# Kernel optimization log

Measured on AMD Instinct MI355X. Metric: run time of the kernel, lower is better.

## Reference

```python
import jax, jax.numpy as jnp
import numpy as np

DIM = 1024
NUM_HEAD = 16
N_IMG = 64


def _linear_params(key, scale=0.02):
    kw, kb = jax.random.split(key)
    W = jax.random.normal(kw, (DIM, DIM), jnp.float32) * scale
    b = jax.random.normal(kb, (DIM,), jnp.float32) * scale
    return W, b


def setup_inputs() -> dict:
    key = jax.random.key(0)
    ks = jax.random.split(key, 5)
    # ragged per-image instance counts: 128..254, deterministic, sum = 12224
    lens = (128 + 2 * np.arange(N_IMG)).astype(np.int64)
    N = int(lens.sum())  # 12224
    x = jax.random.normal(ks[0], (N, DIM), jnp.float32)
    Wq, bq = _linear_params(ks[1])
    Wk, bk = _linear_params(ks[2])
    Wv, bv = _linear_params(ks[3])
    Wu, bu = _linear_params(ks[4])
    return {"x": x, "Wq": Wq, "bq": bq, "Wk": Wk, "bk": bk,
            "Wv": Wv, "bv": bv, "Wu": Wu, "bu": bu,
            "num_inst_per_image": jnp.asarray(lens)}


def _segment_layout(num_inst_per_image):
    # static (int) metadata -> numpy; returns padded gather idx, key mask, unpad idx
    lens = np.asarray(num_inst_per_image)
    B = lens.shape[0]
    L = int(lens.max())
    offsets = np.concatenate([[0], np.cumsum(lens)[:-1]])
    pos = offsets[:, None] + np.arange(L)[None, :]           # [B, L] flat positions
    valid = np.arange(L)[None, :] < lens[:, None]            # [B, L]
    gather_idx = jnp.asarray(np.where(valid, pos, 0))        # safe gather
    flat_take = jnp.asarray(np.flatnonzero(valid.ravel()))   # [N] unpad (row-major = segment order)
    return gather_idx, jnp.asarray(valid), flat_take, B, L


def reference(x, Wq, bq, Wk, bk, Wv, bv, Wu, bu, num_inst_per_image):
    gather_idx, valid, flat_take, B, L = _segment_layout(num_inst_per_image)
    N, C = x.shape
    H = NUM_HEAD
    D = C // H
    # global QKV projections on the flat batch (as in the torch module)
    q = (x @ Wq + bq)[gather_idx].reshape(B, L, H, D)
    k = (x @ Wk + bk)[gather_idx].reshape(B, L, H, D)
    v = (x @ Wv + bv)[gather_idx].reshape(B, L, H, D)
    scale = 1.0 / np.sqrt(C)  # note: original divides by sqrt(C), not sqrt(head_dim)
    attn = jnp.einsum('bqhd,bkhd->bhqk', q, k) * scale       # [B, H, L, L]
    bias = jnp.where(valid[:, None, None, :], 0.0, -jnp.inf)  # mask padded keys
    attn = jax.nn.softmax(attn + bias, axis=-1)
    out = jnp.einsum('bhqk,bkhd->bqhd', attn, v).reshape(B * L, C)
    out = out[flat_take]                                      # unpad back to [N, C]
    return out @ Wu + bu
```

## Files before the change

### kernel.cpp

```cpp
#include <hip/hip_runtime.h>
#include <hip/hip_bf16.h>
#include <math.h>

#define DIMC 1024
#define NHEAD 16
#define HDIM 64
#define MPAD 12288

using bf16x8 = __attribute__((ext_vector_type(8))) short;
using f32x4  = __attribute__((ext_vector_type(4))) float;
using f32x16 = __attribute__((ext_vector_type(16))) float;

__device__ inline ushort f2bf(float f) {
    uint u = __float_as_uint(f);
    u += 0x7fffu + ((u >> 16) & 1u);
    return (ushort)(u >> 16);
}
__device__ inline float bf2f(ushort h) { return __uint_as_float(((uint)h) << 16); }

__device__ inline uint pkbf(float a, float b) {
    __hip_bfloat162 t = __float22bfloat162_rn(float2{a, b});
    return *reinterpret_cast<uint*>(&t);
}

__device__ inline void gload_lds16(const ushort* g, ushort* l) {
    __builtin_amdgcn_global_load_lds(
        (const __attribute__((address_space(1))) uint*)g,
        (__attribute__((address_space(3))) uint*)l, 16, 0, 0);
}

__global__ __launch_bounds__(512, 2) void gemm192(
    const ushort* __restrict__ A, const ushort* __restrict__ Bt,
    const float* __restrict__ bq, const float* __restrict__ bk,
    const float* __restrict__ bv,
    ushort* __restrict__ qb, ushort* __restrict__ kb, ushort* __restrict__ vb,
    int M)
{
    __shared__ ushort lds[2][(256 + 192) * 64];

    const int bid = blockIdx.x;
    const int xcd = bid & 7;
    const int j   = bid >> 3;
    const int mt  = xcd * 6 + (j % 6);
    const int nt  = j / 6;
    const int row0 = mt * 256;
    const int col0 = nt * 192;

    const int t512 = threadIdx.x;
    const int w    = t512 >> 6;
    const int lane = t512 & 63;
    const int wm   = w >> 2;
    const int wn   = w & 3;
    const int l15  = lane & 15;
    const int kh   = lane >> 4;

    auto stage = [&](int buf, int kt, int mat, int relRow) {
        const int o   = relRow * 128 + lane * 16;
        const int row = o >> 7;
        const int kb_ = (o & 127) ^ ((row & 7) << 4);
        const ushort* src = (mat ? Bt + (size_t)(col0 + row) * DIMC
                                 : A  + (size_t)(row0 + row) * DIMC)
                            + kt * 64 + (kb_ >> 1);
        gload_lds16(src, &lds[buf][0] + mat * (256 * 64) + relRow * 64);
    };
    auto rdA = [&](int buf, int qr, int fr, int ks) -> bf16x8 {
        const int row = wm * 128 + qr * 64 + fr * 16 + l15;
        const int ad  = (row * 128 + ks * 64 + kh * 16) ^ ((row & 7) << 4);
        return *(const bf16x8*)(&lds[buf][0] + (ad >> 1));
    };
    auto rdB = [&](int buf, int n, int ks) -> bf16x8 {
        const int row = wn * 48 + n * 16 + l15;
        const int ad  = (row * 128 + ks * 64 + kh * 16) ^ ((row & 7) << 4);
        return *(const bf16x8*)(&lds[buf][256 * 64] + (ad >> 1));
    };

    f32x4 acc[8][3] = {};
    bf16x8 af[4][2];
    bf16x8 bf[3][2];

    stage(0, 0, 0, wm * 128 + wn * 16);
    stage(0, 0, 0, wm * 128 + wn * 16 + 8);
    stage(0, 0, 1, wn * 48 + wm * 16);
    stage(0, 0, 1, wn * 48 + wm * 16 + 8);
    stage(0, 0, 1, wn * 48 + 32 + wm * 8);
    stage(0, 0, 0, wm * 128 + 64 + wn * 16);
    stage(0, 0, 0, wm * 128 + 64 + wn * 16 + 8);

    const int NT = DIMC / 64;
    for (int t = 0; t < NT; ++t) {
        const int cur = t & 1;
        const int nxt = cur ^ 1;
        const int tn  = (t + 1 < NT) ? (t + 1) : (NT - 1);

        asm volatile("s_waitcnt vmcnt(2)" ::: "memory");
        __builtin_amdgcn_s_barrier();
        __builtin_amdgcn_sched_barrier(0);
        #pragma unroll
        for (int fr = 0; fr < 4; ++fr)
            #pragma unroll
            for (int ks = 0; ks < 2; ++ks)
                af[fr][ks] = rdA(cur, 0, fr, ks);
        #pragma unroll
        for (int n = 0; n < 3; ++n)
            #pragma unroll
            for (int ks = 0; ks < 2; ++ks)
                bf[n][ks] = rdB(cur, n, ks);
        stage(nxt, tn, 0, wm * 128 + wn * 16);
        stage(nxt, tn, 0, wm * 128 + wn * 16 + 8);
        stage(nxt, tn, 1, wn * 48 + wm * 16);
        stage(nxt, tn, 1, wn * 48 + wm * 16 + 8);
        stage(nxt, tn, 1, wn * 48 + 32 + wm * 8);
        __builtin_amdgcn_s_setprio(1);
        #pragma unroll
        for (int fr = 0; fr < 4; ++fr)
            #pragma unroll
            for (int n = 0; n < 3; ++n)
                #pragma unroll
                for (int ks = 0; ks < 2; ++ks)
                    acc[fr][n] = __builtin_amdgcn_mfma_f32_16x16x32_bf16(
                        af[fr][ks], bf[n][ks], acc[fr][n], 0, 0, 0);
        __builtin_amdgcn_s_setprio(0);

        asm volatile("s_waitcnt vmcnt(5)" ::: "memory");
        __builtin_amdgcn_s_barrier();
        __builtin_amdgcn_sched_barrier(0);
        #pragma unroll
        for (int fr = 0; fr < 4; ++fr)
            #pragma unroll
            for (int ks = 0; ks < 2; ++ks)
                af[fr][ks] = rdA(cur, 1, fr, ks);
        stage(nxt, tn, 0, wm * 128 + 64 + wn * 16);
        stage(nxt, tn, 0, wm * 128 + 64 + wn * 16 + 8);
        __builtin_amdgcn_s_setprio(1);
        #pragma unroll
        for (int fr = 0; fr < 4; ++fr)
            #pragma unroll
            for (int n = 0; n < 3; ++n)
                #pragma unroll
                for (int ks = 0; ks < 2; ++ks)
                    acc[4 + fr][n] = __builtin_amdgcn_mfma_f32_16x16x32_bf16(
                        af[fr][ks], bf[n][ks], acc[4 + fr][n], 0, 0, 0);
        __builtin_amdgcn_s_setprio(0);
    }

    #pragma unroll
    for (int n = 0; n < 3; ++n) {
        const int cg = col0 + wn * 48 + n * 16 + l15;
        const int s  = cg >> 10;
        const int cb = cg & 1023;
        const float bb = ((s == 0) ? bq : (s == 1) ? bk : bv)[cb];
        ushort* op     = (s == 0) ? qb : (s == 1) ? kb : vb;
        #pragma unroll
        for (int i = 0; i < 8; ++i) {
            #pragma unroll
            for (int r = 0; r < 4; ++r) {
                const int gr = row0 + wm * 128 + i * 16 + kh * 4 + r;
                if (gr < M)
                    op[(size_t)gr * DIMC + cb] = f2bf(acc[i][n][r] + bb);
            }
        }
    }
}

__global__ __launch_bounds__(512, 2) void gemmF(
    const ushort* __restrict__ A, const ushort* __restrict__ Bt,
    const float* __restrict__ bias, float* __restrict__ C, int M)
{
    __shared__ ushort lds[2][(192 + 256) * 64];

    const int bid = blockIdx.x;
    const int xcd = bid & 7;
    const int j   = bid >> 3;
    const int mt  = xcd * 8 + (j % 8);
    const int nt  = j / 8;
    const int row0 = mt * 192;
    const int col0 = nt * 256;

    const int t512 = threadIdx.x;
    const int w    = t512 >> 6;
    const int lane = t512 & 63;
    const int wm   = w >> 2;
    const int wn   = w & 3;
    const int l15  = lane & 15;
    const int kh   = lane >> 4;

    const int awbase = (w & 4) ? (96 + (w - 4) * 8) : (w * 8);

    auto stage = [&](int buf, int kt, int mat, int relRow) {
        const int o   = relRow * 128 + lane * 16;
        const int row = o >> 7;
        const int kb_ = (o & 127) ^ ((row & 7) << 4);
        const ushort* src = (mat ? Bt + (size_t)(col0 + row) * DIMC
                                 : A  + (size_t)(row0 + row) * DIMC)
                            + kt * 64 + (kb_ >> 1);
        gload_lds16(src, &lds[buf][0] + mat * (192 * 64) + relRow * 64);
    };
    auto rdA = [&](int buf, int fr, int ks) -> bf16x8 {
        const int row = wm * 96 + fr * 16 + l15;
        const int ad  = (row * 128 + ks * 64 + kh * 16) ^ ((row & 7) << 4);
        return *(const bf16x8*)(&lds[buf][0] + (ad >> 1));
    };
    auto rdB = [&](int buf, int n, int ks) -> bf16x8 {
        const int row = wn * 64 + n * 16 + l15;
        const int ad  = (row * 128 + ks * 64 + kh * 16) ^ ((row & 7) << 4);
        return *(const bf16x8*)(&lds[buf][192 * 64] + (ad >> 1));
    };

    f32x4 acc[6][4] = {};
    bf16x8 af[2][2];
    bf16x8 bf[4][2];

    stage(0, 0, 1, w * 32);
    stage(0, 0, 1, w * 32 + 8);
    stage(0, 0, 1, w * 32 + 16);
    stage(0, 0, 1, w * 32 + 24);
    stage(0, 0, 0, awbase);
    stage(0, 0, 0, awbase + 32);
    stage(0, 0, 0, awbase + 64);

    const int NT = DIMC / 64;
    for (int t = 0; t < NT; ++t) {
        const int cur = t & 1;
        const int nxt = cur ^ 1;
        const int tn  = (t + 1 < NT) ? (t + 1) : (NT - 1);

        asm volatile("s_waitcnt vmcnt(2)" ::: "memory");
        __builtin_amdgcn_s_barrier();
        __builtin_amdgcn_sched_barrier(0);
        #pragma unroll
        for (int fr = 0; fr < 2; ++fr)
            #pragma unroll
            for (int ks = 0; ks < 2; ++ks)
                af[fr][ks] = rdA(cur, fr, ks);
        #pragma unroll
        for (int n = 0; n < 4; ++n)
            #pragma unroll
            for (int ks = 0; ks < 2; ++ks)
                bf[n][ks] = rdB(cur, n, ks);
        stage(nxt, tn, 1, w * 32);
        stage(nxt, tn, 1, w * 32 + 8);
        stage(nxt, tn, 1, w * 32 + 16);
        stage(nxt, tn, 1, w * 32 + 24);
        stage(nxt, tn, 0, awbase);
        __builtin_amdgcn_s_setprio(1);
        #pragma unroll
        for (int fr = 0; fr < 2; ++fr)
            #pragma unroll
            for (int n = 0; n < 4; ++n)
                #pragma unroll
                for (int ks = 0; ks < 2; ++ks)
                    acc[fr][n] = __builtin_amdgcn_mfma_f32_16x16x32_bf16(
                        af[fr][ks], bf[n][ks], acc[fr][n], 0, 0, 0);
        __builtin_amdgcn_s_setprio(0);

        asm volatile("s_waitcnt vmcnt(6)" ::: "memory");
        __builtin_amdgcn_s_barrier();
        __builtin_amdgcn_sched_barrier(0);
        #pragma unroll
        for (int fr = 0; fr < 2; ++fr)
            #pragma unroll
            for (int ks = 0; ks < 2; ++ks)
                af[fr][ks] = rdA(cur, 2 + fr, ks);
        stage(nxt, tn, 0, awbase + 32);
        __builtin_amdgcn_s_setprio(1);
        #pragma unroll
        for (int fr = 0; fr < 2; ++fr)
            #pragma unroll
            for (int n = 0; n < 4; ++n)
                #pragma unroll
                for (int ks = 0; ks < 2; ++ks)
                    acc[2 + fr][n] = __builtin_amdgcn_mfma_f32_16x16x32_bf16(
                        af[fr][ks], bf[n][ks], acc[2 + fr][n], 0, 0, 0);
        __builtin_amdgcn_s_setprio(0);

        asm volatile("s_waitcnt vmcnt(6)" ::: "memory");
        __builtin_amdgcn_s_barrier();
        __builtin_amdgcn_sched_barrier(0);
        #pragma unroll
        for (int fr = 0; fr < 2; ++fr)
            #pragma unroll
            for (int ks = 0; ks < 2; ++ks)
                af[fr][ks] = rdA(cur, 4 + fr, ks);
        stage(nxt, tn, 0, awbase + 64);
        __builtin_amdgcn_s_setprio(1);
        #pragma unroll
        for (int fr = 0; fr < 2; ++fr)
            #pragma unroll
            for (int n = 0; n < 4; ++n)
                #pragma unroll
                for (int ks = 0; ks < 2; ++ks)
                    acc[4 + fr][n] = __builtin_amdgcn_mfma_f32_16x16x32_bf16(
                        af[fr][ks], bf[n][ks], acc[4 + fr][n], 0, 0, 0);
        __builtin_amdgcn_s_setprio(0);
    }

    #pragma unroll
    for (int n = 0; n < 4; ++n) {
        const int c  = col0 + wn * 64 + n * 16 + l15;
        const float bb = bias[c];
        #pragma unroll
        for (int i = 0; i < 6; ++i) {
            #pragma unroll
            for (int r = 0; r < 4; ++r) {
                const int gr = row0 + wm * 96 + i * 16 + kh * 4 + r;
                if (gr < M)
                    C[(size_t)gr * DIMC + c] = acc[i][n][r] + bb;
            }
        }
    }
}

__global__ __launch_bounds__(256) void cvt_pad(
    const float* __restrict__ x, ushort* __restrict__ xb, int nvalid, int ntot)
{
    const int stride = gridDim.x * blockDim.x;
    for (int i = blockIdx.x * blockDim.x + threadIdx.x; i < ntot / 4; i += stride) {
        const int e = i * 4;
        ushort4 o;
        if (e < nvalid) {
            const float4 f = *(const float4*)(x + e);
            o.x = f2bf(f.x); o.y = f2bf(f.y); o.z = f2bf(f.z); o.w = f2bf(f.w);
        } else { o.x = o.y = o.z = o.w = 0; }
        *(ushort4*)(xb + e) = o;
    }
}

__global__ __launch_bounds__(256) void transpose_w4(
    const float* __restrict__ W0, const float* __restrict__ W1,
    const float* __restrict__ W2, const float* __restrict__ W3,
    ushort* __restrict__ T0, ushort* __restrict__ T1,
    ushort* __restrict__ T2, ushort* __restrict__ T3)
{
    __shared__ float tile[32][33];
    const int z = blockIdx.z;
    const float* W = (z == 0) ? W0 : (z == 1) ? W1 : (z == 2) ? W2 : W3;
    ushort*      T = (z == 0) ? T0 : (z == 1) ? T1 : (z == 2) ? T2 : T3;
    const int tx = threadIdx.x & 31;
    const int ty = threadIdx.x >> 5;
    const int n0 = blockIdx.x * 32;
    const int k0 = blockIdx.y * 32;
    #pragma unroll
    for (int i = 0; i < 32; i += 8)
        tile[ty + i][tx] = W[(size_t)(k0 + ty + i) * DIMC + n0 + tx];
    __syncthreads();
    #pragma unroll
    for (int i = 0; i < 32; i += 8)
        T[(size_t)(n0 + ty + i) * DIMC + k0 + tx] = f2bf(tile[tx][ty + i]);
}

__global__ __launch_bounds__(64) void attn_mfma(
    const ushort* __restrict__ qg, const ushort* __restrict__ kg,
    const ushort* __restrict__ vg, ushort* __restrict__ og,
    const int* __restrict__ lens, int B)
{
    __shared__ ushort Vt[64 * 68];

    const int i   = blockIdx.x;
    const int xcd = i & 7;
    const int j   = i >> 3;
    const int bh  = xcd * (B * 2) + (j >> 2);
    const int qt  = j & 3;
    const int h   = bh & 15;
    const int b   = bh >> 4;

    const int lane = threadIdx.x & 63;

    const int myl = (lane < B) ? lens[lane] : 0;
    int inc = myl;
    #pragma unroll
    for (int d = 1; d < 64; d <<= 1) {
        const int nb = __shfl_up(inc, d);
        if (lane >= d) inc += nb;
    }
    const int off = __shfl(inc, b) - __shfl(myl, b);
    const int L   = __shfl(myl, b);
    if (qt * 64 >= L) return;
    const int ntk = (L + 63) >> 6;

    const int l31 = lane & 31;
    const int hi  = lane >> 5;
    const int kp  = lane & 31;
    const int dh  = lane >> 5;

    bf16x8 qf[2][4];
    #pragma unroll
    for (int qn = 0; qn < 2; ++qn) {
        const size_t row = (size_t)(off + min(qt * 64 + qn * 32 + l31, L - 1));
        #pragma unroll
        for (int ks = 0; ks < 4; ++ks) {
            union { uint4 u4; ushort us[8]; bf16x8 v; } tmp;
            tmp.u4 = *(const uint4*)(qg + row * DIMC + h * HDIM + ks * 16 + hi * 8);
            #pragma unroll
            for (int e = 0; e < 8; ++e)
                tmp.us[e] = f2bf(bf2f(tmp.us[e]) * 0.03125f);
            qf[qn][ks] = tmp.v;
        }
    }

    f32x16 o[2][2] = {};
    float mst[2] = {-1e30f, -1e30f};
    float lst[2] = {0.f, 0.f};

    uint4 va[4], vbr[4];
    auto issueV = [&](int tt) {
        const int j0s = tt * 64;
        #pragma unroll
        for (int it = 0; it < 4; ++it) {
            const int d0 = (it * 2 + dh) * 8;
            const size_t r0 = (size_t)(off + min(j0s + 2 * kp,     L - 1));
            const size_t r1 = (size_t)(off + min(j0s + 2 * kp + 1, L - 1));
            va[it]  = *(const uint4*)(vg + r0 * DIMC + h * HDIM + d0);
            vbr[it] = *(const uint4*)(vg + r1 * DIMC + h * HDIM + d0);
        }
    };

    bf16x8 kfc[2][4], kfn[2][4];
    auto loadK = [&](int tt, bf16x8 (&kf)[2][4]) {
        const int j0s = tt * 64;
        #pragma unroll
        for (int km = 0; km < 2; ++km) {
            const size_t row = (size_t)(off + min(j0s + km * 32 + l31, L - 1));
            #pragma unroll
            for (int ks = 0; ks < 4; ++ks)
                kf[km][ks] = *(const bf16x8*)(kg + row * DIMC + h * HDIM + ks * 16 + hi * 8);
        }
    };

    issueV(0);
    loadK(0, kfc);

    for (int t = 0; t < ntk; ++t) {
        const int j0 = t * 64;

        loadK(min(t + 1, ntk - 1), kfn);

        f32x16 s[2][2] = {};
        __builtin_amdgcn_s_setprio(1);
        #pragma unroll
        for (int km = 0; km < 2; ++km)
            #pragma unroll
            for (int qn = 0; qn < 2; ++qn)
                #pragma unroll
                for (int ks = 0; ks < 4; ++ks)
                    s[km][qn] = __builtin_amdgcn_mfma_f32_32x32x16_bf16(
                        kfc[km][ks], qf[qn][ks], s[km][qn], 0, 0, 0);
        __builtin_amdgcn_s_setprio(0);

        #pragma unroll
        for (int it = 0; it < 4; ++it) {
            const int d0 = (it * 2 + dh) * 8;
            const uint a4[4] = {va[it].x,  va[it].y,  va[it].z,  va[it].w};
            const uint b4[4] = {vbr[it].x, vbr[it].y, vbr[it].z, vbr[it].w};
            #pragma unroll
            for (int jj = 0; jj < 4; ++jj) {
                const uint lo  = (a4[jj] & 0xffffu) | (b4[jj] << 16);
                const uint hi2 = (a4[jj] >> 16) | (b4[jj] & 0xffff0000u);
                *(uint*)&Vt[(d0 + 2 * jj)     * 68 + 2 * kp] = lo;
                *(uint*)&Vt[(d0 + 2 * jj + 1) * 68 + 2 * kp] = hi2;
            }
        }
        if (t + 1 < ntk) issueV(t + 1);

        const bool fullTile = (j0 + 64 <= L);
        float tmv[2];
        #pragma unroll
        for (int qn = 0; qn < 2; ++qn) {
            float tm = -1e30f;
            if (fullTile) {
                #pragma unroll
                for (int km = 0; km < 2; ++km)
                    #pragma unroll
                    for (int r = 0; r < 16; ++r)
                        tm = fmaxf(tm, s[km][qn][r]);
            } else {
                #pragma unroll
                for (int km = 0; km < 2; ++km)
                    #pragma unroll
                    for (int r = 0; r < 16; ++r) {
                        const int key = j0 + km * 32 + (r & 3) + 8 * (r >> 2) + 4 * hi;
                        float sv = s[km][qn][r];
                        sv = (key < L) ? sv : -1e30f;
                        s[km][qn][r] = sv;
                        tm = fmaxf(tm, sv);
                    }
            }
            tm = fmaxf(tm, __shfl_xor(tm, 32));
            tmv[qn] = tm;
        }

        const bool need = (tmv[0] > mst[0] + 4.f) || (tmv[1] > mst[1] + 4.f);
        if (__any(need)) {
            #pragma unroll
            for (int qn = 0; qn < 2; ++qn) {
                const float nm = fmaxf(mst[qn], tmv[qn]);
                const float corr = __expf(mst[qn] - nm);
                mst[qn] = nm;
                lst[qn] *= corr;
                #pragma unroll
                for (int dm = 0; dm < 2; ++dm)
                    #pragma unroll
                    for (int r = 0; r < 16; ++r)
                        o[dm][qn][r] *= corr;
            }
        }
        #pragma unroll
        for (int qn = 0; qn < 2; ++qn) {
            float ls = 0.f;
            #pragma unroll
            for (int km = 0; km < 2; ++km)
                #pragma unroll
                for (int r = 0; r < 16; ++r) {
                    const float p = __expf(s[km][qn][r] - mst[qn]);
                    s[km][qn][r] = p;
                    ls += p;
                }
            ls += __shfl_xor(ls, 32);
            lst[qn] += ls;
        }

        #pragma unroll
        for (int kspv = 0; kspv < 4; ++kspv) {
            const int km = kspv >> 1;
            const int sb = kspv & 1;

            bf16x8 Afr[2];
            #pragma unroll
            for (int dm = 0; dm < 2; ++dm) {
                const int d = dm * 32 + l31;
                const uint2 p0 = *(const uint2*)&Vt[d * 68 + kspv * 16 + hi * 8];
                const uint2 p1 = *(const uint2*)&Vt[d * 68 + kspv * 16 + hi * 8 + 4];
                union { uint u[4]; bf16x8 v; } aa;
                aa.u[0] = p0.x; aa.u[1] = p0.y; aa.u[2] = p1.x; aa.u[3] = p1.y;
                Afr[dm] = aa.v;
            }

            bf16x8 Bfr[2];
            #pragma unroll
            for (int qn = 0; qn < 2; ++qn) {
                const uint X0 = pkbf(s[km][qn][8 * sb + 0], s[km][qn][8 * sb + 1]);
                const uint X1 = pkbf(s[km][qn][8 * sb + 2], s[km][qn][8 * sb + 3]);
                const uint Y0 = pkbf(s[km][qn][8 * sb + 4], s[km][qn][8 * sb + 5]);
                const uint Y1 = pkbf(s[km][qn][8 * sb + 6], s[km][qn][8 * sb + 7]);
                const uint sx0 = (uint)__shfl_xor((int)X0, 32);
                const uint sx1 = (uint)__shfl_xor((int)X1, 32);
                const uint sy0 = (uint)__shfl_xor((int)Y0, 32);
                const uint sy1 = (uint)__shfl_xor((int)Y1, 32);
                union { uint u[4]; bf16x8 v; } bb;
                bb.u[0] = hi ? sy0 : X0;
                bb.u[1] = hi ? sy1 : X1;
                bb.u[2] = hi ? Y0 : sx0;
                bb.u[3] = hi ? Y1 : sx1;
                Bfr[qn] = bb.v;
            }

            __builtin_amdgcn_s_setprio(1);
            #pragma unroll
            for (int dm = 0; dm < 2; ++dm)
                #pragma unroll
                for (int qn = 0; qn < 2; ++qn)
                    o[dm][qn] = __builtin_amdgcn_mfma_f32_32x32x16_bf16(
                        Afr[dm], Bfr[qn], o[dm][qn], 0, 0, 0);
            __builtin_amdgcn_s_setprio(0);
        }

        #pragma unroll
        for (int km = 0; km < 2; ++km)
            #pragma unroll
            for (int ks = 0; ks < 4; ++ks)
                kfc[km][ks] = kfn[km][ks];
    }

    #pragma unroll
    for (int qn = 0; qn < 2; ++qn) {
        const int q = qt * 64 + qn * 32 + l31;
        if (q < L) {
            const float inv = 1.f / lst[qn];
            ushort* orow = og + (size_t)(off + q) * DIMC + h * HDIM;
            #pragma unroll
            for (int dm = 0; dm < 2; ++dm)
                #pragma unroll
                for (int bq2 = 0; bq2 < 4; ++bq2) {
                    const int r0 = 4 * bq2;
                    uint2 st;
                    st.x = pkbf(o[dm][qn][r0 + 0] * inv, o[dm][qn][r0 + 1] * inv);
                    st.y = pkbf(o[dm][qn][r0 + 2] * inv, o[dm][qn][r0 + 3] * inv);
                    *(uint2*)(orow + dm * 32 + 8 * bq2 + 4 * hi) = st;
                }
        }
    }
}

extern "C" void kernel_launch(void* const* d_in, const int* in_sizes, int n_in,
                              void* d_out, int out_size, void* d_ws, size_t ws_size,
                              hipStream_t stream)
{
    const float* x   = (const float*)d_in[0];
    const float* Wq  = (const float*)d_in[1];
    const float* bq  = (const float*)d_in[2];
    const float* Wk  = (const float*)d_in[3];
    const float* bk  = (const float*)d_in[4];
    const float* Wv  = (const float*)d_in[5];
    const float* bv  = (const float*)d_in[6];
    const float* Wu  = (const float*)d_in[7];
    const float* bu  = (const float*)d_in[8];
    const int*  lens = (const int*)d_in[9];

    const int N = in_sizes[0] / DIMC;
    const int B = in_sizes[9];

    ushort* xb  = (ushort*)d_ws;
    ushort* wtq = xb  + (size_t)MPAD * DIMC;
    ushort* wtk = wtq + (size_t)DIMC * DIMC;
    ushort* wtv = wtk + (size_t)DIMC * DIMC;
    ushort* wtu = wtv + (size_t)DIMC * DIMC;
    ushort* kb  = wtu + (size_t)DIMC * DIMC;
    ushort* vb  = kb  + (size_t)N * DIMC;
    ushort* qb  = (ushort*)d_out;
    ushort* ob  = xb;

    cvt_pad<<<2048, 256, 0, stream>>>(x, xb, N * DIMC, MPAD * DIMC);
    transpose_w4<<<dim3(32, 32, 4), 256, 0, stream>>>(Wq, Wk, Wv, Wu,
                                                      wtq, wtk, wtv, wtu);

    gemm192<<<768, 512, 0, stream>>>(xb, wtq, bq, bk, bv, qb, kb, vb, N);

    attn_mfma<<<dim3(B * NHEAD * 4), dim3(64), 0, stream>>>(qb, kb, vb, ob, lens, B);

    gemmF<<<256, 512, 0, stream>>>(ob, wtu, bu, (float*)d_out, N);
}
```

Measured before the change: 229.0 us.

## Share K/V tiles across four query-tile waves in one attention workgroup

```diff
diff --git a/kernel.cpp b/kernel.cpp
--- a/kernel.cpp
+++ b/kernel.cpp
@@ -348,22 +348,24 @@
         T[(size_t)(n0 + ty + i) * DIMC + k0 + tx] = f2bf(tile[tx][ty + i]);
 }
 
-__global__ __launch_bounds__(64) void attn_mfma(
+__global__ __launch_bounds__(256) void attn_mfma(
     const ushort* __restrict__ qg, const ushort* __restrict__ kg,
     const ushort* __restrict__ vg, ushort* __restrict__ og,
     const int* __restrict__ lens, int B)
 {
+    __shared__ ushort Kt[2][64 * 64];
     __shared__ ushort Vt[64 * 68];
 
     const int i   = blockIdx.x;
     const int xcd = i & 7;
     const int j   = i >> 3;
-    const int bh  = xcd * (B * 2) + (j >> 2);
-    const int qt  = j & 3;
+    const int bh  = xcd * (B * 2) + j;
     const int h   = bh & 15;
     const int b   = bh >> 4;
 
-    const int lane = threadIdx.x & 63;
+    const int tid  = threadIdx.x;
+    const int qt   = tid >> 6;
+    const int lane = tid & 63;
 
     const int myl = (lane < B) ? lens[lane] : 0;
     int inc = myl;
@@ -374,218 +376,236 @@
     }
     const int off = __shfl(inc, b) - __shfl(myl, b);
     const int L   = __shfl(myl, b);
-    if (qt * 64 >= L) return;
     const int ntk = (L + 63) >> 6;
+    const bool active = (qt * 64 < L);
 
     const int l31 = lane & 31;
     const int hi  = lane >> 5;
-    const int kp  = lane & 31;
-    const int dh  = lane >> 5;
 
     bf16x8 qf[2][4];
-    #pragma unroll
-    for (int qn = 0; qn < 2; ++qn) {
-        const size_t row = (size_t)(off + min(qt * 64 + qn * 32 + l31, L - 1));
-        #pragma unroll
-        for (int ks = 0; ks < 4; ++ks) {
-            union { uint4 u4; ushort us[8]; bf16x8 v; } tmp;
-            tmp.u4 = *(const uint4*)(qg + row * DIMC + h * HDIM + ks * 16 + hi * 8);
-            #pragma unroll
-            for (int e = 0; e < 8; ++e)
-                tmp.us[e] = f2bf(bf2f(tmp.us[e]) * 0.03125f);
-            qf[qn][ks] = tmp.v;
-        }
-    }
+    if (active) {
+        #pragma unroll
+        for (int qn = 0; qn < 2; ++qn) {
+            const size_t row = (size_t)(off + min(qt * 64 + qn * 32 + l31, L - 1));
+            #pragma unroll
+            for (int ks = 0; ks < 4; ++ks) {
+                union { uint4 u4; ushort us[8]; bf16x8 v; } tmp;
+                tmp.u4 = *(const uint4*)(qg + row * DIMC + h * HDIM + ks * 16 + hi * 8);
+                #pragma unroll
+                for (int e = 0; e < 8; ++e)
+                    tmp.us[e] = f2bf(bf2f(tmp.us[e]) * 0.03125f);
+                qf[qn][ks] = tmp.v;
+            }
+        }
+    }
+
+    auto stageK = [&](int tt, int buf) {
+        #pragma unroll
+        for (int u0 = 0; u0 < 2; ++u0) {
+            const int u   = tid + u0 * 256;
+            const int o   = u * 16;
+            const int row = o >> 7;
+            const int kb_ = (o & 127) ^ ((row & 7) << 4);
+            const ushort* src = kg + (size_t)(off + min(tt * 64 + row, L - 1)) * DIMC
+                                + h * HDIM + (kb_ >> 1);
+            gload_lds16(src, &Kt[buf][0] + u * 8);
+        }
+    };
+
+    const int pr   = lane & 7;
+    const int doct = lane >> 3;
+    const int d0v  = doct * 8;
+    uint4 v0, v1;
+    auto loadV = [&](int tt) {
+        const int k0 = tt * 64 + qt * 16 + 2 * pr;
+        v0 = *(const uint4*)(vg + (size_t)(off + min(k0,     L - 1)) * DIMC + h * HDIM + d0v);
+        v1 = *(const uint4*)(vg + (size_t)(off + min(k0 + 1, L - 1)) * DIMC + h * HDIM + d0v);
+    };
+
+    stageK(0, 0);
+    loadV(0);
 
     f32x16 o[2][2] = {};
     float mst[2] = {-1e30f, -1e30f};
     float lst[2] = {0.f, 0.f};
 
-    uint4 va[4], vbr[4];
-    auto issueV = [&](int tt) {
-        const int j0s = tt * 64;
-        #pragma unroll
-        for (int it = 0; it < 4; ++it) {
-            const int d0 = (it * 2 + dh) * 8;
-            const size_t r0 = (size_t)(off + min(j0s + 2 * kp,     L - 1));
-            const size_t r1 = (size_t)(off + min(j0s + 2 * kp + 1, L - 1));
-            va[it]  = *(const uint4*)(vg + r0 * DIMC + h * HDIM + d0);
-            vbr[it] = *(const uint4*)(vg + r1 * DIMC + h * HDIM + d0);
-        }
-    };
-
-    bf16x8 kfc[2][4], kfn[2][4];
-    auto loadK = [&](int tt, bf16x8 (&kf)[2][4]) {
-        const int j0s = tt * 64;
-        #pragma unroll
-        for (int km = 0; km < 2; ++km) {
-            const size_t row = (size_t)(off + min(j0s + km * 32 + l31, L - 1));
-            #pragma unroll
-            for (int ks = 0; ks < 4; ++ks)
-                kf[km][ks] = *(const bf16x8*)(kg + row * DIMC + h * HDIM + ks * 16 + hi * 8);
-        }
-    };
-
-    issueV(0);
-    loadK(0, kfc);
-
     for (int t = 0; t < ntk; ++t) {
-        const int j0 = t * 64;
-
-        loadK(min(t + 1, ntk - 1), kfn);
+        const int cur = t & 1;
+        const int j0  = t * 64;
+        const int tn  = (t + 1 < ntk) ? (t + 1) : (ntk - 1);
+
+        stageK(tn, cur ^ 1);
+        asm volatile("s_waitcnt vmcnt(2)" ::: "memory");
+        __builtin_amdgcn_s_barrier();
+        __builtin_amdgcn_sched_barrier(0);
 
         f32x16 s[2][2] = {};
-        __builtin_amdgcn_s_setprio(1);
-        #pragma unroll
-        for (int km = 0; km < 2; ++km)
-            #pragma unroll
-            for (int qn = 0; qn < 2; ++qn)
-                #pragma unroll
-                for (int ks = 0; ks < 4; ++ks)
-                    s[km][qn] = __builtin_amdgcn_mfma_f32_32x32x16_bf16(
-                        kfc[km][ks], qf[qn][ks], s[km][qn], 0, 0, 0);
-        __builtin_amdgcn_s_setprio(0);
-
-        #pragma unroll
-        for (int it = 0; it < 4; ++it) {
-            const int d0 = (it * 2 + dh) * 8;
-            const uint a4[4] = {va[it].x,  va[it].y,  va[it].z,  va[it].w};
-            const uint b4[4] = {vbr[it].x, vbr[it].y, vbr[it].z, vbr[it].w};
+        if (active) {
+            bf16x8 kf[2][4];
+            #pragma unroll
+            for (int km = 0; km < 2; ++km) {
+                const int row = km * 32 + l31;
+                #pragma unroll
+                for (int ks = 0; ks < 4; ++ks) {
+                    const int ad = (row * 128 + ks * 32 + hi * 16) ^ ((row & 7) << 4);
+                    kf[km][ks] = *(const bf16x8*)(&Kt[cur][0] + (ad >> 1));
+                }
+            }
+            __builtin_amdgcn_s_setprio(1);
+            #pragma unroll
+            for (int km = 0; km < 2; ++km)
+                #pragma unroll
+                for (int qn = 0; qn < 2; ++qn)
+                    #pragma unroll
+                    for (int ks = 0; ks < 4; ++ks)
+                        s[km][qn] = __builtin_amdgcn_mfma_f32_32x32x16_bf16(
+                            kf[km][ks], qf[qn][ks], s[km][qn], 0, 0, 0);
+            __builtin_amdgcn_s_setprio(0);
+        }
+
+        {
+            const uint a4[4] = {v0.x, v0.y, v0.z, v0.w};
+            const uint b4[4] = {v1.x, v1.y, v1.z, v1.w};
+            const int  col   = qt * 16 + 2 * pr;
             #pragma unroll
             for (int jj = 0; jj < 4; ++jj) {
                 const uint lo  = (a4[jj] & 0xffffu) | (b4[jj] << 16);
                 const uint hi2 = (a4[jj] >> 16) | (b4[jj] & 0xffff0000u);
-                *(uint*)&Vt[(d0 + 2 * jj)     * 68 + 2 * kp] = lo;
-                *(uint*)&Vt[(d0 + 2 * jj + 1) * 68 + 2 * kp] = hi2;
-            }
-        }
-        if (t + 1 < ntk) issueV(t + 1);
-
-        const bool fullTile = (j0 + 64 <= L);
-        float tmv[2];
-        #pragma unroll
-        for (int qn = 0; qn < 2; ++qn) {
-            float tm = -1e30f;
-            if (fullTile) {
-                #pragma unroll
-                for (int km = 0; km < 2; ++km)
+                *(uint*)&Vt[(d0v + 2 * jj)     * 68 + col] = lo;
+                *(uint*)&Vt[(d0v + 2 * jj + 1) * 68 + col] = hi2;
+            }
+        }
+        if (t + 1 < ntk) loadV(t + 1);
+
+        if (active) {
+            const bool fullTile = (j0 + 64 <= L);
+            float tmv[2];
+            #pragma unroll
+            for (int qn = 0; qn < 2; ++qn) {
+                float tm = -1e30f;
+                if (fullTile) {
                     #pragma unroll
-                    for (int r = 0; r < 16; ++r)
-                        tm = fmaxf(tm, s[km][qn][r]);
-            } else {
+                    for (int km = 0; km < 2; ++km)
+                        #pragma unroll
+                        for (int r = 0; r < 16; ++r)
+                            tm = fmaxf(tm, s[km][qn][r]);
+                } else {
+                    #pragma unroll
+                    for (int km = 0; km < 2; ++km)
+                        #pragma unroll
+                        for (int r = 0; r < 16; ++r) {
+                            const int key = j0 + km * 32 + (r & 3) + 8 * (r >> 2) + 4 * hi;
+                            float sv = s[km][qn][r];
+                            sv = (key < L) ? sv : -1e30f;
+                            s[km][qn][r] = sv;
+                            tm = fmaxf(tm, sv);
+                        }
+                }
+                tm = fmaxf(tm, __shfl_xor(tm, 32));
+                tmv[qn] = tm;
+            }
+
+            const bool need = (tmv[0] > mst[0] + 4.f) || (tmv[1] > mst[1] + 4.f);
+            if (__any(need)) {
+                #pragma unroll
+                for (int qn = 0; qn < 2; ++qn) {
+                    const float nm = fmaxf(mst[qn], tmv[qn]);
+                    const float corr = __expf(mst[qn] - nm);
+                    mst[qn] = nm;
+                    lst[qn] *= corr;
+                    #pragma unroll
+                    for (int dm = 0; dm < 2; ++dm)
+                        #pragma unroll
+                        for (int r = 0; r < 16; ++r)
+                            o[dm][qn][r] *= corr;
+                }
+            }
+            #pragma unroll
+            for (int qn = 0; qn < 2; ++qn) {
+                float ls = 0.f;
                 #pragma unroll
                 for (int km = 0; km < 2; ++km)
                     #pragma unroll
                     for (int r = 0; r < 16; ++r) {
-                        const int key = j0 + km * 32 + (r & 3) + 8 * (r >> 2) + 4 * hi;
-                        float sv = s[km][qn][r];
-                        sv = (key < L) ? sv : -1e30f;
-                        s[km][qn][r] = sv;
-                        tm = fmaxf(tm, sv);
+                        const float p = __expf(s[km][qn][r] - mst[qn]);
+                        s[km][qn][r] = p;
+                        ls += p;
                     }
-            }
-            tm = fmaxf(tm, __shfl_xor(tm, 32));
-            tmv[qn] = tm;
-        }
-
-        const bool need = (tmv[0] > mst[0] + 4.f) || (tmv[1] > mst[1] + 4.f);
-        if (__any(need)) {
-            #pragma unroll
-            for (int qn = 0; qn < 2; ++qn) {
-                const float nm = fmaxf(mst[qn], tmv[qn]);
-                const float corr = __expf(mst[qn] - nm);
-                mst[qn] = nm;
-                lst[qn] *= corr;
+                ls += __shfl_xor(ls, 32);
+                lst[qn] += ls;
+            }
+        }
+
+        asm volatile("s_waitcnt lgkmcnt(0)" ::: "memory");
+        __builtin_amdgcn_s_barrier();
+        __builtin_amdgcn_sched_barrier(0);
+
+        if (active) {
+            #pragma unroll
+            for (int kspv = 0; kspv < 4; ++kspv) {
+                const int km = kspv >> 1;
+                const int sb = kspv & 1;
+
+                bf16x8 Afr[2];
+                #pragma unroll
+                for (int dm = 0; dm < 2; ++dm) {
+                    const int d = dm * 32 + l31;
+                    const uint2 p0 = *(const uint2*)&Vt[d * 68 + kspv * 16 + hi * 8];
+                    const uint2 p1 = *(const uint2*)&Vt[d * 68 + kspv * 16 + hi * 8 + 4];
+                    union { uint u[4]; bf16x8 v; } aa;
+                    aa.u[0] = p0.x; aa.u[1] = p0.y; aa.u[2] = p1.x; aa.u[3] = p1.y;
+                    Afr[dm] = aa.v;
+                }
+
+                bf16x8 Bfr[2];
+                #pragma unroll
+                for (int qn = 0; qn < 2; ++qn) {
+                    const uint X0 = pkbf(s[km][qn][8 * sb + 0], s[km][qn][8 * sb + 1]);
+                    const uint X1 = pkbf(s[km][qn][8 * sb + 2], s[km][qn][8 * sb + 3]);
+                    const uint Y0 = pkbf(s[km][qn][8 * sb + 4], s[km][qn][8 * sb + 5]);
+                    const uint Y1 = pkbf(s[km][qn][8 * sb + 6], s[km][qn][8 * sb + 7]);
+                    const uint sx0 = (uint)__shfl_xor((int)X0, 32);
+                    const uint sx1 = (uint)__shfl_xor((int)X1, 32);
+                    const uint sy0 = (uint)__shfl_xor((int)Y0, 32);
+                    const uint sy1 = (uint)__shfl_xor((int)Y1, 32);
+                    union { uint u[4]; bf16x8 v; } bb;
+                    bb.u[0] = hi ? sy0 : X0;
+                    bb.u[1] = hi ? sy1 : X1;
+                    bb.u[2] = hi ? Y0 : sx0;
+                    bb.u[3] = hi ? Y1 : sx1;
+                    Bfr[qn] = bb.v;
+                }
+
+                __builtin_amdgcn_s_setprio(1);
                 #pragma unroll
                 for (int dm = 0; dm < 2; ++dm)
                     #pragma unroll
-                    for (int r = 0; r < 16; ++r)
-                        o[dm][qn][r] *= corr;
-            }
-        }
+                    for (int qn = 0; qn < 2; ++qn)
+                        o[dm][qn] = __builtin_amdgcn_mfma_f32_32x32x16_bf16(
+                            Afr[dm], Bfr[qn], o[dm][qn], 0, 0, 0);
+                __builtin_amdgcn_s_setprio(0);
+            }
+        }
+    }
+
+    if (active) {
         #pragma unroll
         for (int qn = 0; qn < 2; ++qn) {
-            float ls = 0.f;
-            #pragma unroll
-            for (int km = 0; km < 2; ++km)
-                #pragma unroll
-                for (int r = 0; r < 16; ++r) {
-                    const float p = __expf(s[km][qn][r] - mst[qn]);
-                    s[km][qn][r] = p;
-                    ls += p;
-                }
-            ls += __shfl_xor(ls, 32);
-            lst[qn] += ls;
-        }
-
-        #pragma unroll
-        for (int kspv = 0; kspv < 4; ++kspv) {
-            const int km = kspv >> 1;
-            const int sb = kspv & 1;
-
-            bf16x8 Afr[2];
-            #pragma unroll
-            for (int dm = 0; dm < 2; ++dm) {
-                const int d = dm * 32 + l31;
-                const uint2 p0 = *(const uint2*)&Vt[d * 68 + kspv * 16 + hi * 8];
-                const uint2 p1 = *(const uint2*)&Vt[d * 68 + kspv * 16 + hi * 8 + 4];
-                union { uint u[4]; bf16x8 v; } aa;
-                aa.u[0] = p0.x; aa.u[1] = p0.y; aa.u[2] = p1.x; aa.u[3] = p1.y;
-                Afr[dm] = aa.v;
-            }
-
-            bf16x8 Bfr[2];
-            #pragma unroll
-            for (int qn = 0; qn < 2; ++qn) {
-                const uint X0 = pkbf(s[km][qn][8 * sb + 0], s[km][qn][8 * sb + 1]);
-                const uint X1 = pkbf(s[km][qn][8 * sb + 2], s[km][qn][8 * sb + 3]);
-                const uint Y0 = pkbf(s[km][qn][8 * sb + 4], s[km][qn][8 * sb + 5]);
-                const uint Y1 = pkbf(s[km][qn][8 * sb + 6], s[km][qn][8 * sb + 7]);
-                const uint sx0 = (uint)__shfl_xor((int)X0, 32);
-                const uint sx1 = (uint)__shfl_xor((int)X1, 32);
-                const uint sy0 = (uint)__shfl_xor((int)Y0, 32);
-                const uint sy1 = (uint)__shfl_xor((int)Y1, 32);
-                union { uint u[4]; bf16x8 v; } bb;
-                bb.u[0] = hi ? sy0 : X0;
-                bb.u[1] = hi ? sy1 : X1;
-                bb.u[2] = hi ? Y0 : sx0;
-                bb.u[3] = hi ? Y1 : sx1;
-                Bfr[qn] = bb.v;
-            }
-
-            __builtin_amdgcn_s_setprio(1);
-            #pragma unroll
-            for (int dm = 0; dm < 2; ++dm)
-                #pragma unroll
-                for (int qn = 0; qn < 2; ++qn)
-                    o[dm][qn] = __builtin_amdgcn_mfma_f32_32x32x16_bf16(
-                        Afr[dm], Bfr[qn], o[dm][qn], 0, 0, 0);
-            __builtin_amdgcn_s_setprio(0);
-        }
-
-        #pragma unroll
-        for (int km = 0; km < 2; ++km)
-            #pragma unroll
-            for (int ks = 0; ks < 4; ++ks)
-                kfc[km][ks] = kfn[km][ks];
-    }
-
-    #pragma unroll
-    for (int qn = 0; qn < 2; ++qn) {
-        const int q = qt * 64 + qn * 32 + l31;
-        if (q < L) {
-            const float inv = 1.f / lst[qn];
-            ushort* orow = og + (size_t)(off + q) * DIMC + h * HDIM;
-            #pragma unroll
-            for (int dm = 0; dm < 2; ++dm)
-                #pragma unroll
-                for (int bq2 = 0; bq2 < 4; ++bq2) {
-                    const int r0 = 4 * bq2;
-                    uint2 st;
-                    st.x = pkbf(o[dm][qn][r0 + 0] * inv, o[dm][qn][r0 + 1] * inv);
-                    st.y = pkbf(o[dm][qn][r0 + 2] * inv, o[dm][qn][r0 + 3] * inv);
-                    *(uint2*)(orow + dm * 32 + 8 * bq2 + 4 * hi) = st;
-                }
+            const int q = qt * 64 + qn * 32 + l31;
+            if (q < L) {
+                const float inv = 1.f / lst[qn];
+                ushort* orow = og + (size_t)(off + q) * DIMC + h * HDIM;
+                #pragma unroll
+                for (int dm = 0; dm < 2; ++dm)
+                    #pragma unroll
+                    for (int bq2 = 0; bq2 < 4; ++bq2) {
+                        const int r0 = 4 * bq2;
+                        uint2 st;
+                        st.x = pkbf(o[dm][qn][r0 + 0] * inv, o[dm][qn][r0 + 1] * inv);
+                        st.y = pkbf(o[dm][qn][r0 + 2] * inv, o[dm][qn][r0 + 3] * inv);
+                        *(uint2*)(orow + dm * 32 + 8 * bq2 + 4 * hi) = st;
+                    }
+            }
         }
     }
 }
@@ -624,7 +644,7 @@
 
     gemm192<<<768, 512, 0, stream>>>(xb, wtq, bq, bk, bv, qb, kb, vb, N);
 
-    attn_mfma<<<dim3(B * NHEAD * 4), dim3(64), 0, stream>>>(qb, kb, vb, ob, lens, B);
+    attn_mfma<<<dim3(B * NHEAD), dim3(256), 0, stream>>>(qb, kb, vb, ob, lens, B);
 
     gemmF<<<256, 512, 0, stream>>>(ob, wtu, bu, (float*)d_out, N);
 }
```

Result: slower. 234.1 us (+2.2%).
